# Kernel optimization log

Hardware: AMD Instinct MI355X
Metric: run time of the kernel (lower is better)

The kernel has to match this reference:

```python
import jax, jax.numpy as jnp
from jax import lax
import numpy as np

K = 3  # kernel size for both convs


def setup_inputs() -> dict:
    key = jax.random.key(0)
    k1, k2, k3, k4, k5 = jax.random.split(key, 5)
    x = jax.random.normal(k1, (8, 3, 384, 384), dtype=jnp.float32)
    # offset-producing conv: 18 = 2*3*3 offset channels for a 3x3 deform kernel
    w1 = jax.random.normal(k2, (18, 3, K, K), dtype=jnp.float32) * 0.05
    b1 = jax.random.normal(k3, (18,), dtype=jnp.float32) * 0.05
    # deformable conv weight/bias: in=3, out=3, 3x3
    w2 = jax.random.normal(k4, (3, 3, K, K), dtype=jnp.float32) * 0.2
    b2 = jax.random.normal(k5, (3,), dtype=jnp.float32) * 0.05
    return {"x": x, "w1": w1, "b1": b1, "w2": w2, "b2": b2}


def _deform_conv2d(x, offset, w, b):
    # x: [B,C,H,W], offset: [B, 2*K*K, Ho, Wo] (per-tap (dy,dx) interleaved),
    # w: [Co,C,K,K], b: [Co]. stride=1, pad=0, dilation=1, zero-padding bilinear.
    B, C, H, W = x.shape
    KK = K * K
    Ho, Wo = H - (K - 1), W - (K - 1)
    off = offset.reshape(B, KK, 2, Ho, Wo)
    dy, dx = off[:, :, 0], off[:, :, 1]                      # [B,KK,Ho,Wo]

    kh = jnp.repeat(jnp.arange(K, dtype=jnp.float32), K)     # [KK] kernel row
    kw = jnp.tile(jnp.arange(K, dtype=jnp.float32), K)       # [KK] kernel col
    base_y = jnp.arange(Ho, dtype=jnp.float32)[None, :, None] + kh[:, None, None]  # [KK,Ho,1]
    base_x = jnp.arange(Wo, dtype=jnp.float32)[None, None, :] + kw[:, None, None]  # [KK,1,Wo]
    py = base_y[None] + dy                                   # [B,KK,Ho,Wo]
    px = base_x[None] + dx

    y0 = jnp.floor(py)
    x0 = jnp.floor(px)
    wy = py - y0
    wx = px - x0

    x_flat = x.reshape(B, C, H * W)
    N = KK * Ho * Wo

    def gather_corner(yc, xc, wgt):
        valid = (yc >= 0) & (yc <= H - 1) & (xc >= 0) & (xc <= W - 1)
        yi = jnp.clip(yc, 0, H - 1).astype(jnp.int32)
        xi = jnp.clip(xc, 0, W - 1).astype(jnp.int32)
        idx = (yi * W + xi).reshape(B, 1, N)
        g = jnp.take_along_axis(x_flat, idx, axis=2)          # [B,C,N]
        return g * (wgt * valid.astype(x.dtype)).reshape(B, 1, N)

    val = gather_corner(y0, x0, (1 - wy) * (1 - wx))
    val = val + gather_corner(y0, x0 + 1, (1 - wy) * wx)
    val = val + gather_corner(y0 + 1, x0, wy * (1 - wx))
    val = val + gather_corner(y0 + 1, x0 + 1, wy * wx)
    val = val.reshape(B, C, KK, Ho, Wo)

    out = jnp.einsum('bckhw,ock->bohw', val, w.reshape(w.shape[0], C, KK))
    return out + b[None, :, None, None]


def reference(x, w1, b1, w2, b2):
    offset = lax.conv_general_dilated(
        x, w1, window_strides=(1, 1), padding='VALID',
        dimension_numbers=('NCHW', 'OIHW', 'NCHW')) + b1[None, :, None, None]
    return _deform_conv2d(x, offset, w2, b2)
```

## Files before the change

kernel.cpp:

```cpp
#include <hip/hip_runtime.h>


#define BB 8
#define HH 384
#define WW 384
#define HO 382
#define WO 382
#define HW (HH * WW)
#define TW 32
#define TH 8
#define TILES_X 12
#define TILES_Y 48
#define SROWS 15
#define SCOLS 39
#define SSTRIDE 39

#define WS_W1P 0
#define WS_W2P 512
#define WS_W2S 576
#define WS_FLOATS 640

typedef float v2f __attribute__((ext_vector_type(2), aligned(8)));
typedef float v4f __attribute__((ext_vector_type(4), aligned(16)));

static __device__ __forceinline__ v2f fma2(v2f a, v2f b, v2f c) {
    return __builtin_elementwise_fma(a, b, c);
}
static __device__ __forceinline__ v2f lo2(v4f v) { v2f r; r.x = v.x; r.y = v.y; return r; }
static __device__ __forceinline__ v2f hi2(v4f v) { v2f r; r.x = v.z; r.y = v.w; return r; }
static __device__ __forceinline__ v2f bc2(float f) { v2f r; r.x = f; r.y = f; return r; }

__global__ __launch_bounds__(512) void prep_weights(
    const float* __restrict__ w1,
    const float* __restrict__ w2,
    float* __restrict__ ws)
{
    const int i = threadIdx.x;
    if (i < 486) {
        const int oc = i / 27, rem = i % 27, c = rem / 9, j = rem % 9;
        const int k = oc >> 1, comp = oc & 1;
        ws[WS_W1P + ((j * 3 + c) * 9 + k) * 2 + comp] = w1[i];
    }
    if (i < 81) {
        const int o = i / 27, c = (i % 27) / 9, k = i % 9;
        if (o < 2) ws[WS_W2P + (k * 3 + c) * 2 + o] = w2[i];
        else       ws[WS_W2S + k * 3 + c] = w2[i];
    }
}

template<bool USE_WS>
__global__ __launch_bounds__(256, 4) void deform_tiled(
    const float* __restrict__ x,
    const float* __restrict__ w1,
    const float* __restrict__ b1,
    const float* __restrict__ w2,
    const float* __restrict__ b2,
    const float* __restrict__ wsp,
    float* __restrict__ out)
{
    __shared__ v4f  s_p01[SROWS * SSTRIDE];
    __shared__ v2f  s_p2 [SROWS * SSTRIDE];
    __shared__ float s_w1p[486];
    __shared__ float s_w2p[54];
    __shared__ float s_w2s[27];

    if constexpr (!USE_WS) {
        for (int i = threadIdx.x; i < 486; i += 256) {
            const int oc = i / 27, rem = i % 27, c = rem / 9, j = rem % 9;
            const int k = oc >> 1, comp = oc & 1;
            s_w1p[((j * 3 + c) * 9 + k) * 2 + comp] = w1[i];
        }
        if (threadIdx.x < 81) {
            const int i = threadIdx.x;
            const int o = i / 27, c = (i % 27) / 9, k = i % 9;
            if (o < 2) s_w2p[(k * 3 + c) * 2 + o] = w2[i];
            else       s_w2s[k * 3 + c] = w2[i];
        }
    }

    const v2f*   __restrict__ w1p;
    const v2f*   __restrict__ w2p;
    const float* __restrict__ w2s;
    if constexpr (USE_WS) {
        w1p = (const v2f*)(wsp + WS_W1P);
        w2p = (const v2f*)(wsp + WS_W2P);
        w2s = wsp + WS_W2S;
    } else {
        w1p = (const v2f*)s_w1p;
        w2p = (const v2f*)s_w2p;
        w2s = s_w2s;
    }

    const int b  = blockIdx.x & 7;
    const int t  = blockIdx.x >> 3;
    const int tx = t % TILES_X;
    const int ty = t / TILES_X;
    const int w0 = tx * TW;
    const int r0 = ty * TH;

    const float* xp0 = x + (long)b * 3 * HW;
    const float* xp1 = xp0 + HW;
    const float* xp2 = xp0 + 2 * HW;

    const int gr0 = r0 - 2, gc0 = w0 - 2;
    for (int s = threadIdx.x; s < SROWS * SCOLS; s += 256) {
        const int sr = s / SCOLS, sc = s - sr * SCOLS;
        const int gy = min(max(gr0 + sr, 0), HH - 1);
        const int gx = min(max(gc0 + sc, 0), WW - 1);
        const int base = gy * WW + gx;
        const float c0 = xp0[base];
        const float c1 = xp1[base];
        const float c2 = xp2[base];
        v2f p; p.x = c0; p.y = c1;
        const int e = sr * SSTRIDE + sc;
        *(v2f*)(&s_p01[e]) = p;
        s_p2[e].x = c2;
        if (sc > 0) {
            *((v2f*)(&s_p01[e - 1]) + 1) = p;
            s_p2[e - 1].y = c2;
        }
    }
    __syncthreads();

    const int wo_in = threadIdx.x & 31;
    const int ho_in = threadIdx.x >> 5;
    const int wo = w0 + wo_in;
    const int ho = r0 + ho_in;
    if (wo >= WO || ho >= HO) return;

    v2f off2[9];
    const v2f* __restrict__ b1p = (const v2f*)b1;
#pragma unroll
    for (int k = 0; k < 9; ++k) off2[k] = b1p[k];

    const int pc = wo_in + 2;
#pragma unroll
    for (int i = 0; i < 3; ++i) {
        const int rowb = (ho_in + 2 + i) * SSTRIDE + pc;
        const v4f pa = s_p01[rowb];
        const v4f pb = s_p01[rowb + 2];
        const v2f sa = s_p2[rowb];
        const v2f sb = s_p2[rowb + 2];
        const float xs0[3] = { pa.x, pa.y, sa.x };
        const float xs1[3] = { pa.z, pa.w, sa.y };
        const float xs2[3] = { pb.x, pb.y, sb.x };
#pragma unroll
        for (int jj = 0; jj < 3; ++jj) {
            const int j = i * 3 + jj;
#pragma unroll
            for (int c = 0; c < 3; ++c) {
                const float xc = (jj == 0) ? xs0[c] : (jj == 1) ? xs1[c] : xs2[c];
                const v2f xcv = bc2(xc);
                const v2f* wrow = w1p + (j * 3 + c) * 9;
#pragma unroll
                for (int k = 0; k < 9; ++k)
                    off2[k] = fma2(xcv, wrow[k], off2[k]);
            }
        }
    }

    float acc0 = b2[0], acc1 = b2[1], acc2 = b2[2];

    const bool interior = (gr0 >= 0) & (gc0 >= 0) &
                          (gr0 + SROWS <= HH) & (gc0 + SCOLS <= WW);

    if (interior) {
        unsigned bad = 0u;
        int ibv[9];
        v2f frv[9];
#pragma unroll
        for (int k = 0; k < 9; ++k) {
            const int kh = k / 3, kw = k - kh * 3;
            v2f pos; pos.x = (float)(ho + kh); pos.y = (float)(wo + kw);
            pos += off2[k];
            const v2f fl = __builtin_elementwise_floor(pos);
            frv[k] = pos - fl;
            const int y0 = (int)fl.x;
            const int x0 = (int)fl.y;
            const int ly0 = y0 - gr0;
            const int lx  = x0 - gc0;

            bad |= (((unsigned)ly0 > (unsigned)(SROWS - 2)) |
                    ((unsigned)lx  > (unsigned)(SCOLS - 2))) ? (1u << k) : 0u;

            const int cy0 = min(max(ly0, 0), SROWS - 2);
            const int cx  = min(max(lx, 0),  SCOLS - 2);
            ibv[k] = cy0 * SSTRIDE + cx;
        }

#pragma unroll
        for (int k = 0; k < 9; ++k) {
            const int ib = ibv[k];
            const v4f r0v = s_p01[ib];
            const v4f r1v = s_p01[ib + SSTRIDE];
            const v2f s0v = s_p2[ib];
            const v2f s1v = s_p2[ib + SSTRIDE];

            const v2f fr = frv[k];
            const float g00 = (1.f - fr.x) * (1.f - fr.y);
            const float g01 = (1.f - fr.x) * fr.y;
            const float g10 = fr.x * (1.f - fr.y);
            const float g11 = fr.x * fr.y;

            v2f t01 = bc2(g00) * lo2(r0v);
            t01 = fma2(bc2(g01), hi2(r0v), t01);
            t01 = fma2(bc2(g10), lo2(r1v), t01);
            t01 = fma2(bc2(g11), hi2(r1v), t01);
            float t2 = g00 * s0v.x;
            t2 = fmaf(g01, s0v.y, t2);
            t2 = fmaf(g10, s1v.x, t2);
            t2 = fmaf(g11, s1v.y, t2);

            const float v0 = t01.x, v1 = t01.y, v2v = t2;

            v2f acc01; acc01.x = acc0; acc01.y = acc1;
            acc01 = fma2(bc2(v0),  w2p[k * 3 + 0], acc01);
            acc01 = fma2(bc2(v1),  w2p[k * 3 + 1], acc01);
            acc01 = fma2(bc2(v2v), w2p[k * 3 + 2], acc01);
            acc0 = acc01.x; acc1 = acc01.y;
            acc2 = fmaf(w2s[k * 3 + 0], v0, acc2);
            acc2 = fmaf(w2s[k * 3 + 1], v1, acc2);
            acc2 = fmaf(w2s[k * 3 + 2], v2v, acc2);
        }

        if (bad) {
#pragma unroll 1
            for (int k = 0; k < 9; ++k) {
                if ((bad >> k) & 1u) {
                    const int kh = k / 3, kw = k - kh * 3;
                    v2f pos; pos.x = (float)(ho + kh); pos.y = (float)(wo + kw);
                    pos += off2[k];
                    const v2f fl = __builtin_elementwise_floor(pos);
                    const v2f fr = pos - fl;
                    const int y0 = (int)fl.x;
                    const int x0 = (int)fl.y;

                    const int ly0 = y0 - gr0;
                    const int lx  = x0 - gc0;
                    const float a00 = (1.f - fr.x) * (1.f - fr.y);
                    const float a01 = (1.f - fr.x) * fr.y;
                    const float a10 = fr.x * (1.f - fr.y);
                    const float a11 = fr.x * fr.y;
                    const int cy0 = min(max(ly0, 0), SROWS - 2);
                    const int cx  = min(max(lx, 0),  SCOLS - 2);
                    const int ib  = cy0 * SSTRIDE + cx;
                    const v4f r0v = s_p01[ib];
                    const v4f r1v = s_p01[ib + SSTRIDE];
                    const v2f s0v = s_p2[ib];
                    const v2f s1v = s_p2[ib + SSTRIDE];
                    v2f tw01 = bc2(a00) * lo2(r0v);
                    tw01 = fma2(bc2(a01), hi2(r0v), tw01);
                    tw01 = fma2(bc2(a10), lo2(r1v), tw01);
                    tw01 = fma2(bc2(a11), hi2(r1v), tw01);
                    float tw2 = a00 * s0v.x;
                    tw2 = fmaf(a01, s0v.y, tw2);
                    tw2 = fmaf(a10, s1v.x, tw2);
                    tw2 = fmaf(a11, s1v.y, tw2);

                    const int ry0 = min(max(y0, 0), HH - 1);
                    const int ry1 = min(max(y0 + 1, 0), HH - 1);
                    const int xbs = min(max(x0, 0), WW - 2);
                    const bool vy0 = (y0 >= 0) & (y0 <= HH - 1);
                    const bool vy1 = (y0 >= -1) & (y0 <= HH - 2);
                    const bool vx0 = (x0 >= 0) & (x0 <= WW - 1);
                    const bool vx1 = (x0 >= -1) & (x0 <= WW - 2);
                    const float wy0m = vy0 ? (1.f - fr.x) : 0.f;
                    const float wy1m = vy1 ? fr.x : 0.f;
                    const float wx0m = vx0 ? (1.f - fr.y) : 0.f;
                    const float wx1m = vx1 ? fr.y : 0.f;
                    const bool selA = (x0 >= WW - 1);
                    const bool selB = (x0 >= 0);
                    const float e0 = (selA ? 0.f : wx0m) + (selB ? 0.f : wx1m);
                    const float e1 = (selA ? wx0m : 0.f) + (selB ? wx1m : 0.f);
                    const float g00 = wy0m * e0, g01 = wy0m * e1;
                    const float g10 = wy1m * e0, g11 = wy1m * e1;
                    const int o0 = ry0 * WW + xbs;
                    const int o1 = ry1 * WW + xbs;
                    v4f r0g, r1g; v2f s0g, s1g;
                    r0g.x = xp0[o0];     r0g.y = xp1[o0];
                    r0g.z = xp0[o0 + 1]; r0g.w = xp1[o0 + 1];
                    s0g.x = xp2[o0];     s0g.y = xp2[o0 + 1];
                    r1g.x = xp0[o1];     r1g.y = xp1[o1];
                    r1g.z = xp0[o1 + 1]; r1g.w = xp1[o1 + 1];
                    s1g.x = xp2[o1];     s1g.y = xp2[o1 + 1];
                    v2f tr01 = bc2(g00) * lo2(r0g);
                    tr01 = fma2(bc2(g01), hi2(r0g), tr01);
                    tr01 = fma2(bc2(g10), lo2(r1g), tr01);
                    tr01 = fma2(bc2(g11), hi2(r1g), tr01);
                    float tr2 = g00 * s0g.x;
                    tr2 = fmaf(g01, s0g.y, tr2);
                    tr2 = fmaf(g10, s1g.x, tr2);
                    tr2 = fmaf(g11, s1g.y, tr2);

                    const float d0 = tr01.x - tw01.x;
                    const float d1 = tr01.y - tw01.y;
                    const float d2 = tr2 - tw2;

                    v2f acc01; acc01.x = acc0; acc01.y = acc1;
                    acc01 = fma2(bc2(d0), w2p[k * 3 + 0], acc01);
                    acc01 = fma2(bc2(d1), w2p[k * 3 + 1], acc01);
                    acc01 = fma2(bc2(d2), w2p[k * 3 + 2], acc01);
                    acc0 = acc01.x; acc1 = acc01.y;
                    acc2 = fmaf(w2s[k * 3 + 0], d0, acc2);
                    acc2 = fmaf(w2s[k * 3 + 1], d1, acc2);
                    acc2 = fmaf(w2s[k * 3 + 2], d2, acc2);
                }
            }
        }
    } else {
#pragma unroll 1
        for (int k = 0; k < 9; ++k) {
            const int kh = k / 3, kw = k - kh * 3;
            v2f pos; pos.x = (float)(ho + kh); pos.y = (float)(wo + kw);
            pos += off2[k];
            const v2f fl = __builtin_elementwise_floor(pos);
            const v2f fr = pos - fl;
            const int y0 = (int)fl.x;
            const int x0 = (int)fl.y;

            const int ry0 = min(max(y0, 0), HH - 1);
            const int ry1 = min(max(y0 + 1, 0), HH - 1);
            const int xbs = min(max(x0, 0), WW - 2);

            const bool vy0 = (y0 >= 0) & (y0 <= HH - 1);
            const bool vy1 = (y0 >= -1) & (y0 <= HH - 2);
            const bool vx0 = (x0 >= 0) & (x0 <= WW - 1);
            const bool vx1 = (x0 >= -1) & (x0 <= WW - 2);
            const float wy0m = vy0 ? (1.f - fr.x) : 0.f;
            const float wy1m = vy1 ? fr.x : 0.f;
            const float wx0m = vx0 ? (1.f - fr.y) : 0.f;
            const float wx1m = vx1 ? fr.y : 0.f;

            const bool selA = (x0 >= WW - 1);
            const bool selB = (x0 >= 0);
            const float e0 = (selA ? 0.f : wx0m) + (selB ? 0.f : wx1m);
            const float e1 = (selA ? wx0m : 0.f) + (selB ? wx1m : 0.f);
            const float g00 = wy0m * e0, g01 = wy0m * e1;
            const float g10 = wy1m * e0, g11 = wy1m * e1;

            const int ly0 = ry0 - gr0;
            const int ly1 = ry1 - gr0;
            const int lx  = xbs - gc0;
            const bool inTile = ((unsigned)ly0 <= SROWS - 1) &
                                ((unsigned)ly1 <= SROWS - 1) &
                                ((unsigned)lx  <= SCOLS - 2);

            const int cy0 = min(max(ly0, 0), SROWS - 1);
            const int cy1 = min(max(ly1, 0), SROWS - 1);
            const int cx  = min(max(lx, 0),  SCOLS - 2);
            const int ib0 = cy0 * SSTRIDE + cx;
            const int ib1 = cy1 * SSTRIDE + cx;
            v4f r0v = s_p01[ib0];
            v4f r1v = s_p01[ib1];
            v2f s0v = s_p2[ib0];
            v2f s1v = s_p2[ib1];

            if (!inTile) {
                const int o0 = ry0 * WW + xbs;
                const int o1 = ry1 * WW + xbs;
                r0v.x = xp0[o0];     r0v.y = xp1[o0];
                r0v.z = xp0[o0 + 1]; r0v.w = xp1[o0 + 1];
                s0v.x = xp2[o0];     s0v.y = xp2[o0 + 1];
                r1v.x = xp0[o1];     r1v.y = xp1[o1];
                r1v.z = xp0[o1 + 1]; r1v.w = xp1[o1 + 1];
                s1v.x = xp2[o1];     s1v.y = xp2[o1 + 1];
            }

            v2f t01 = bc2(g00) * lo2(r0v);
            t01 = fma2(bc2(g01), hi2(r0v), t01);
            t01 = fma2(bc2(g10), lo2(r1v), t01);
            t01 = fma2(bc2(g11), hi2(r1v), t01);
            float t2 = g00 * s0v.x;
            t2 = fmaf(g01, s0v.y, t2);
            t2 = fmaf(g10, s1v.x, t2);
            t2 = fmaf(g11, s1v.y, t2);

            const float v0 = t01.x, v1 = t01.y, v2v = t2;

            v2f acc01; acc01.x = acc0; acc01.y = acc1;
            acc01 = fma2(bc2(v0),  w2p[k * 3 + 0], acc01);
            acc01 = fma2(bc2(v1),  w2p[k * 3 + 1], acc01);
            acc01 = fma2(bc2(v2v), w2p[k * 3 + 2], acc01);
            acc0 = acc01.x; acc1 = acc01.y;
            acc2 = fmaf(w2s[k * 3 + 0], v0, acc2);
            acc2 = fmaf(w2s[k * 3 + 1], v1, acc2);
            acc2 = fmaf(w2s[k * 3 + 2], v2v, acc2);
        }
    }

    const long obase = ((long)(b * 3) * HO + ho) * WO + wo;
    __builtin_nontemporal_store(acc0, out + obase);
    __builtin_nontemporal_store(acc1, out + obase + (long)HO * WO);
    __builtin_nontemporal_store(acc2, out + obase + 2L * HO * WO);
}

extern "C" void kernel_launch(void* const* d_in, const int* in_sizes, int n_in,
                              void* d_out, int out_size, void* d_ws, size_t ws_size,
                              hipStream_t stream) {
    const float* x  = (const float*)d_in[0];
    const float* w1 = (const float*)d_in[1];
    const float* b1 = (const float*)d_in[2];
    const float* w2 = (const float*)d_in[3];
    const float* b2 = (const float*)d_in[4];
    float* out = (float*)d_out;
    float* ws  = (float*)d_ws;

    const int blocks = TILES_X * TILES_Y * BB;
    const bool use_ws = (d_ws != nullptr) && (ws_size >= WS_FLOATS * sizeof(float));

    if (use_ws) {
        prep_weights<<<1, 512, 0, stream>>>(w1, w2, ws);
        deform_tiled<true><<<blocks, 256, 0, stream>>>(x, w1, b1, w2, b2, ws, out);
    } else {
        deform_tiled<false><<<blocks, 256, 0, stream>>>(x, w1, b1, w2, b2, nullptr, out);
    }
}
```

Baseline: 105.8 us.

## Repack input to channel-interleaved float4 and gather bilinear taps from global

```diff
diff --git a/kernel.cpp b/kernel.cpp
--- a/kernel.cpp
+++ b/kernel.cpp
@@ -18,17 +18,55 @@
 #define WS_W1P 0
 #define WS_W2P 512
 #define WS_W2S 576
-#define WS_FLOATS 640
+#define WS_X4  640
+#define WS_WEIGHT_FLOATS 640
+#define WS_FAST_FLOATS (WS_X4 + 8L * HW * 4)
 
 typedef float v2f __attribute__((ext_vector_type(2), aligned(8)));
 typedef float v4f __attribute__((ext_vector_type(4), aligned(16)));
 
 static __device__ __forceinline__ v2f fma2(v2f a, v2f b, v2f c) {
+    return __builtin_elementwise_fma(a, b, c);
+}
+static __device__ __forceinline__ v4f fma4(v4f a, v4f b, v4f c) {
     return __builtin_elementwise_fma(a, b, c);
 }
 static __device__ __forceinline__ v2f lo2(v4f v) { v2f r; r.x = v.x; r.y = v.y; return r; }
 static __device__ __forceinline__ v2f hi2(v4f v) { v2f r; r.x = v.z; r.y = v.w; return r; }
 static __device__ __forceinline__ v2f bc2(float f) { v2f r; r.x = f; r.y = f; return r; }
+static __device__ __forceinline__ v4f bc4(float f) { v4f r; r.x = f; r.y = f; r.z = f; r.w = f; return r; }
+
+__global__ __launch_bounds__(256) void prep_fast(
+    const float* __restrict__ x,
+    const float* __restrict__ w1,
+    const float* __restrict__ w2,
+    float* __restrict__ ws)
+{
+    const int bid = blockIdx.x;
+    if (bid == 0) {
+        for (int i = threadIdx.x; i < 486; i += 256) {
+            const int oc = i / 27, rem = i % 27, c = rem / 9, j = rem % 9;
+            const int k = oc >> 1, comp = oc & 1;
+            ws[WS_W1P + ((j * 3 + c) * 9 + k) * 2 + comp] = w1[i];
+        }
+        if (threadIdx.x < 81) {
+            const int i = threadIdx.x;
+            const int o = i / 27, c = (i % 27) / 9, k = i % 9;
+            if (o < 2) ws[WS_W2P + (k * 3 + c) * 2 + o] = w2[i];
+            else       ws[WS_W2S + k * 3 + c] = w2[i];
+        }
+    }
+    const int b = bid & 7;
+    const int chunk = bid >> 3;
+    const int p = chunk * 256 + (int)threadIdx.x;
+    const float* xb = x + (long)b * 3 * HW;
+    v4f q;
+    q.x = xb[p];
+    q.y = xb[p + HW];
+    q.z = xb[p + 2 * HW];
+    q.w = 0.f;
+    *(v4f*)(ws + WS_X4 + ((long)b * HW + p) * 4) = q;
+}
 
 __global__ __launch_bounds__(512) void prep_weights(
     const float* __restrict__ w1,
@@ -46,6 +84,184 @@
         if (o < 2) ws[WS_W2P + (k * 3 + c) * 2 + o] = w2[i];
         else       ws[WS_W2S + k * 3 + c] = w2[i];
     }
+}
+
+__global__ __launch_bounds__(256, 4) void deform_gather(
+    const float* __restrict__ x,
+    const float* __restrict__ b1,
+    const float* __restrict__ b2,
+    const float* __restrict__ wsp,
+    float* __restrict__ out)
+{
+    const v2f*   __restrict__ w1p = (const v2f*)(wsp + WS_W1P);
+    const v2f*   __restrict__ w2p = (const v2f*)(wsp + WS_W2P);
+    const float* __restrict__ w2s = wsp + WS_W2S;
+
+    const int b  = blockIdx.x & 7;
+    const int t  = blockIdx.x >> 3;
+    const int tx = t % TILES_X;
+    const int ty = t / TILES_X;
+    const int wo = tx * TW + (int)(threadIdx.x & 31);
+    const int ho = ty * TH + (int)(threadIdx.x >> 5);
+    if (wo >= WO || ho >= HO) return;
+
+    const v4f* __restrict__ xq = (const v4f*)(wsp + WS_X4) + (long)b * HW;
+    const float* xp0 = x + (long)b * 3 * HW;
+    const float* xp1 = xp0 + HW;
+    const float* xp2 = xp0 + 2 * HW;
+
+    v2f off2[9];
+    const v2f* __restrict__ b1p = (const v2f*)b1;
+#pragma unroll
+    for (int k = 0; k < 9; ++k) off2[k] = b1p[k];
+
+#pragma unroll
+    for (int i = 0; i < 3; ++i) {
+        const int rb = (ho + i) * WW + wo;
+        const v4f qa = xq[rb];
+        const v4f qb = xq[rb + 1];
+        const v4f qc = xq[rb + 2];
+        const float xs0[3] = { qa.x, qa.y, qa.z };
+        const float xs1[3] = { qb.x, qb.y, qb.z };
+        const float xs2[3] = { qc.x, qc.y, qc.z };
+#pragma unroll
+        for (int jj = 0; jj < 3; ++jj) {
+            const int j = i * 3 + jj;
+#pragma unroll
+            for (int c = 0; c < 3; ++c) {
+                const float xc = (jj == 0) ? xs0[c] : (jj == 1) ? xs1[c] : xs2[c];
+                const v2f xcv = bc2(xc);
+                const v2f* wrow = w1p + (j * 3 + c) * 9;
+#pragma unroll
+                for (int k = 0; k < 9; ++k)
+                    off2[k] = fma2(xcv, wrow[k], off2[k]);
+            }
+        }
+    }
+
+    float acc0 = b2[0], acc1 = b2[1], acc2 = b2[2];
+    unsigned bad = 0u;
+    int pv[9];
+    v2f frv[9];
+#pragma unroll
+    for (int k = 0; k < 9; ++k) {
+        const int kh = k / 3, kw = k - kh * 3;
+        v2f pos; pos.x = (float)(ho + kh); pos.y = (float)(wo + kw);
+        pos += off2[k];
+        const v2f fl = __builtin_elementwise_floor(pos);
+        frv[k] = pos - fl;
+        const int y0 = (int)fl.x;
+        const int x0 = (int)fl.y;
+        bad |= (((unsigned)y0 > (unsigned)(HH - 2)) |
+                ((unsigned)x0 > (unsigned)(WW - 2))) ? (1u << k) : 0u;
+        const int cy = min(max(y0, 0), HH - 2);
+        const int cx = min(max(x0, 0), WW - 2);
+        pv[k] = cy * WW + cx;
+    }
+
+#pragma unroll
+    for (int k = 0; k < 9; ++k) {
+        const v4f* p0 = xq + pv[k];
+        const v4f q00 = p0[0], q01 = p0[1];
+        const v4f q10 = p0[WW], q11 = p0[WW + 1];
+
+        const v2f fr = frv[k];
+        const float g00 = (1.f - fr.x) * (1.f - fr.y);
+        const float g01 = (1.f - fr.x) * fr.y;
+        const float g10 = fr.x * (1.f - fr.y);
+        const float g11 = fr.x * fr.y;
+
+        v4f t4 = bc4(g00) * q00;
+        t4 = fma4(bc4(g01), q01, t4);
+        t4 = fma4(bc4(g10), q10, t4);
+        t4 = fma4(bc4(g11), q11, t4);
+        const float v0 = t4.x, v1 = t4.y, v2v = t4.z;
+
+        v2f acc01; acc01.x = acc0; acc01.y = acc1;
+        acc01 = fma2(bc2(v0),  w2p[k * 3 + 0], acc01);
+        acc01 = fma2(bc2(v1),  w2p[k * 3 + 1], acc01);
+        acc01 = fma2(bc2(v2v), w2p[k * 3 + 2], acc01);
+        acc0 = acc01.x; acc1 = acc01.y;
+        acc2 = fmaf(w2s[k * 3 + 0], v0, acc2);
+        acc2 = fmaf(w2s[k * 3 + 1], v1, acc2);
+        acc2 = fmaf(w2s[k * 3 + 2], v2v, acc2);
+    }
+
+    if (bad) {
+#pragma unroll 1
+        for (int k = 0; k < 9; ++k) {
+            if ((bad >> k) & 1u) {
+                const int kh = k / 3, kw = k - kh * 3;
+                v2f pos; pos.x = (float)(ho + kh); pos.y = (float)(wo + kw);
+                pos += off2[k];
+                const v2f fl = __builtin_elementwise_floor(pos);
+                const v2f fr = pos - fl;
+                const int y0 = (int)fl.x;
+                const int x0 = (int)fl.y;
+
+                const int cy = min(max(y0, 0), HH - 2);
+                const int cx = min(max(x0, 0), WW - 2);
+                const v4f* p0 = xq + (cy * WW + cx);
+                const v4f w00 = p0[0], w01 = p0[1];
+                const v4f w10 = p0[WW], w11 = p0[WW + 1];
+                const float a00 = (1.f - fr.x) * (1.f - fr.y);
+                const float a01 = (1.f - fr.x) * fr.y;
+                const float a10 = fr.x * (1.f - fr.y);
+                const float a11 = fr.x * fr.y;
+                v4f tw = bc4(a00) * w00;
+                tw = fma4(bc4(a01), w01, tw);
+                tw = fma4(bc4(a10), w10, tw);
+                tw = fma4(bc4(a11), w11, tw);
+
+                const int ry0 = min(max(y0, 0), HH - 1);
+                const int ry1 = min(max(y0 + 1, 0), HH - 1);
+                const int xbs = min(max(x0, 0), WW - 2);
+                const bool vy0 = (y0 >= 0) & (y0 <= HH - 1);
+                const bool vy1 = (y0 >= -1) & (y0 <= HH - 2);
+                const bool vx0 = (x0 >= 0) & (x0 <= WW - 1);
+                const bool vx1 = (x0 >= -1) & (x0 <= WW - 2);
+                const float wy0m = vy0 ? (1.f - fr.x) : 0.f;
+                const float wy1m = vy1 ? fr.x : 0.f;
+                const float wx0m = vx0 ? (1.f - fr.y) : 0.f;
+                const float wx1m = vx1 ? fr.y : 0.f;
+                const bool selA = (x0 >= WW - 1);
+                const bool selB = (x0 >= 0);
+                const float e0 = (selA ? 0.f : wx0m) + (selB ? 0.f : wx1m);
+                const float e1 = (selA ? wx0m : 0.f) + (selB ? wx1m : 0.f);
+                const float g00 = wy0m * e0, g01 = wy0m * e1;
+                const float g10 = wy1m * e0, g11 = wy1m * e1;
+                const int o0 = ry0 * WW + xbs;
+                const int o1 = ry1 * WW + xbs;
+                v4f r0g, r1g, r2g, r3g;
+                r0g.x = xp0[o0];     r0g.y = xp1[o0];     r0g.z = xp2[o0];     r0g.w = 0.f;
+                r1g.x = xp0[o0 + 1]; r1g.y = xp1[o0 + 1]; r1g.z = xp2[o0 + 1]; r1g.w = 0.f;
+                r2g.x = xp0[o1];     r2g.y = xp1[o1];     r2g.z = xp2[o1];     r2g.w = 0.f;
+                r3g.x = xp0[o1 + 1]; r3g.y = xp1[o1 + 1]; r3g.z = xp2[o1 + 1]; r3g.w = 0.f;
+                v4f tr = bc4(g00) * r0g;
+                tr = fma4(bc4(g01), r1g, tr);
+                tr = fma4(bc4(g10), r2g, tr);
+                tr = fma4(bc4(g11), r3g, tr);
+
+                const float d0 = tr.x - tw.x;
+                const float d1 = tr.y - tw.y;
+                const float d2 = tr.z - tw.z;
+
+                v2f acc01; acc01.x = acc0; acc01.y = acc1;
+                acc01 = fma2(bc2(d0), w2p[k * 3 + 0], acc01);
+                acc01 = fma2(bc2(d1), w2p[k * 3 + 1], acc01);
+                acc01 = fma2(bc2(d2), w2p[k * 3 + 2], acc01);
+                acc0 = acc01.x; acc1 = acc01.y;
+                acc2 = fmaf(w2s[k * 3 + 0], d0, acc2);
+                acc2 = fmaf(w2s[k * 3 + 1], d1, acc2);
+                acc2 = fmaf(w2s[k * 3 + 2], d2, acc2);
+            }
+        }
+    }
+
+    const long obase = ((long)(b * 3) * HO + ho) * WO + wo;
+    __builtin_nontemporal_store(acc0, out + obase);
+    __builtin_nontemporal_store(acc1, out + obase + (long)HO * WO);
+    __builtin_nontemporal_store(acc2, out + obase + 2L * HO * WO);
 }
 
 template<bool USE_WS>
@@ -179,10 +395,8 @@
             const int x0 = (int)fl.y;
             const int ly0 = y0 - gr0;
             const int lx  = x0 - gc0;
-
             bad |= (((unsigned)ly0 > (unsigned)(SROWS - 2)) |
                     ((unsigned)lx  > (unsigned)(SCOLS - 2))) ? (1u << k) : 0u;
-
             const int cy0 = min(max(ly0, 0), SROWS - 2);
             const int cx  = min(max(lx, 0),  SCOLS - 2);
             ibv[k] = cy0 * SSTRIDE + cx;
@@ -195,13 +409,11 @@
             const v4f r1v = s_p01[ib + SSTRIDE];
             const v2f s0v = s_p2[ib];
             const v2f s1v = s_p2[ib + SSTRIDE];
-
             const v2f fr = frv[k];
             const float g00 = (1.f - fr.x) * (1.f - fr.y);
             const float g01 = (1.f - fr.x) * fr.y;
             const float g10 = fr.x * (1.f - fr.y);
             const float g11 = fr.x * fr.y;
-
             v2f t01 = bc2(g00) * lo2(r0v);
             t01 = fma2(bc2(g01), hi2(r0v), t01);
             t01 = fma2(bc2(g10), lo2(r1v), t01);
@@ -210,9 +422,7 @@
             t2 = fmaf(g01, s0v.y, t2);
             t2 = fmaf(g10, s1v.x, t2);
             t2 = fmaf(g11, s1v.y, t2);
-
             const float v0 = t01.x, v1 = t01.y, v2v = t2;
-
             v2f acc01; acc01.x = acc0; acc01.y = acc1;
             acc01 = fma2(bc2(v0),  w2p[k * 3 + 0], acc01);
             acc01 = fma2(bc2(v1),  w2p[k * 3 + 1], acc01);
@@ -234,7 +444,6 @@
                     const v2f fr = pos - fl;
                     const int y0 = (int)fl.x;
                     const int x0 = (int)fl.y;
-
                     const int ly0 = y0 - gr0;
                     const int lx  = x0 - gc0;
                     const float a00 = (1.f - fr.x) * (1.f - fr.y);
@@ -321,7 +530,6 @@
             const int ry0 = min(max(y0, 0), HH - 1);
             const int ry1 = min(max(y0 + 1, 0), HH - 1);
             const int xbs = min(max(x0, 0), WW - 2);
-
             const bool vy0 = (y0 >= 0) & (y0 <= HH - 1);
             const bool vy1 = (y0 >= -1) & (y0 <= HH - 2);
             const bool vx0 = (x0 >= 0) & (x0 <= WW - 1);
@@ -330,7 +538,6 @@
             const float wy1m = vy1 ? fr.x : 0.f;
             const float wx0m = vx0 ? (1.f - fr.y) : 0.f;
             const float wx1m = vx1 ? fr.y : 0.f;
-
             const bool selA = (x0 >= WW - 1);
             const bool selB = (x0 >= 0);
             const float e0 = (selA ? 0.f : wx0m) + (selB ? 0.f : wx1m);
@@ -344,7 +551,6 @@
             const bool inTile = ((unsigned)ly0 <= SROWS - 1) &
                                 ((unsigned)ly1 <= SROWS - 1) &
                                 ((unsigned)lx  <= SCOLS - 2);
-
             const int cy0 = min(max(ly0, 0), SROWS - 1);
             const int cy1 = min(max(ly1, 0), SROWS - 1);
             const int cx  = min(max(lx, 0),  SCOLS - 2);
@@ -354,7 +560,6 @@
             v4f r1v = s_p01[ib1];
             v2f s0v = s_p2[ib0];
             v2f s1v = s_p2[ib1];
-
             if (!inTile) {
                 const int o0 = ry0 * WW + xbs;
                 const int o1 = ry1 * WW + xbs;
@@ -365,7 +570,6 @@
                 r1v.z = xp0[o1 + 1]; r1v.w = xp1[o1 + 1];
                 s1v.x = xp2[o1];     s1v.y = xp2[o1 + 1];
             }
-
             v2f t01 = bc2(g00) * lo2(r0v);
             t01 = fma2(bc2(g01), hi2(r0v), t01);
             t01 = fma2(bc2(g10), lo2(r1v), t01);
@@ -374,9 +578,7 @@
             t2 = fmaf(g01, s0v.y, t2);
             t2 = fmaf(g10, s1v.x, t2);
             t2 = fmaf(g11, s1v.y, t2);
-
             const float v0 = t01.x, v1 = t01.y, v2v = t2;
-
             v2f acc01; acc01.x = acc0; acc01.y = acc1;
             acc01 = fma2(bc2(v0),  w2p[k * 3 + 0], acc01);
             acc01 = fma2(bc2(v1),  w2p[k * 3 + 1], acc01);
@@ -406,9 +608,11 @@
     float* ws  = (float*)d_ws;
 
     const int blocks = TILES_X * TILES_Y * BB;
-    const bool use_ws = (d_ws != nullptr) && (ws_size >= WS_FLOATS * sizeof(float));
-
-    if (use_ws) {
+
+    if (ws != nullptr && ws_size >= (size_t)WS_FAST_FLOATS * sizeof(float)) {
+        prep_fast<<<4608, 256, 0, stream>>>(x, w1, w2, ws);
+        deform_gather<<<blocks, 256, 0, stream>>>(x, b1, b2, ws, out);
+    } else if (ws != nullptr && ws_size >= (size_t)WS_WEIGHT_FLOATS * sizeof(float)) {
         prep_weights<<<1, 512, 0, stream>>>(w1, w2, ws);
         deform_tiled<true><<<blocks, 256, 0, stream>>>(x, w1, b1, w2, b2, ws, out);
     } else {
```

Result: slower. 126.0 us (+19.1%).
